# Kernel optimization log

Measured on AMD Instinct MI355X. Metric: run time of the kernel, lower is better.

The kernel has to match this reference:

```python
import jax, jax.numpy as jnp
import numpy as np

NUM_ITERS = 10  # forward() runs power_iteration with num_iters=10


def setup_inputs() -> dict:
    key = jax.random.key(0)
    k1, k2 = jax.random.split(key)
    out_ch, in_ch, h, w = 2048, 2048, 3, 3
    conv_filter = jax.random.normal(k1, (out_ch, in_ch, h, w), dtype=jnp.float32) * 0.02
    u = jax.random.normal(k2, (1, in_ch * w), dtype=jnp.float32)
    u = u / jnp.linalg.norm(u, axis=1, keepdims=True)
    return {"conv_filter": conv_filter, "u": u}


def reference(conv_filter, u):
    out_ch, in_ch, h, w = conv_filter.shape
    # permute (0,2,1,3) then view as [out_ch*h, in_ch*w]
    W = jnp.transpose(conv_filter, (0, 2, 1, 3)).reshape(out_ch * h, in_ch * w)
    Ws = jax.lax.stop_gradient(W)  # power iteration vectors are detached

    def body(i, carry):
        u_n, _ = carry
        v = u_n @ Ws.T                                   # [1, out_ch*h]
        v_n = v / jnp.linalg.norm(v, axis=1, keepdims=True)
        u2 = v_n @ Ws                                    # [1, in_ch*w]
        u_n2 = u2 / jnp.linalg.norm(u2, axis=1, keepdims=True)
        return (u_n2, v_n)

    v0 = jnp.zeros((1, out_ch * h), dtype=conv_filter.dtype)  # overwritten in first iter
    u_n, v_n = jax.lax.fori_loop(0, NUM_ITERS, body, (u, v0))

    # sigma = v W u^T with u, v treated as constants (custom autograd Function)
    sigma = (v_n @ W) @ u_n.T                            # [1, 1]
    return jnp.sqrt(jnp.asarray(h * w, dtype=conv_filter.dtype)) * sigma
```

## Files before the change

### kernel.cpp

```cpp
#include <hip/hip_runtime.h>
#include <hip/hip_bf16.h>
#include <hip/hip_fp16.h>

#define OC_N     2048
#define IC_N     2048
#define RC       6144
#define OCSTRIDE 18432
#define UNSCALE  0.0000152587890625f

typedef float v2f __attribute__((ext_vector_type(2)));

__device__ __forceinline__ float wave_reduce(float x) {
#pragma unroll
    for (int off = 32; off > 0; off >>= 1) x += __shfl_down(x, off, 64);
    return x;
}

__global__ __launch_bounds__(256) void convert_q_kernel(
    const float* __restrict__ conv, unsigned char* __restrict__ Wq)
{
    const int t  = blockIdx.x * 256 + threadIdx.x;
    const int o8 = t * 8;
    const int r  = o8 / RC;
    const int c0 = o8 % RC;
    const int oc = r / 3, hh = r % 3;
    const float* base = conv + (size_t)oc * OCSTRIDE + hh * 3;
    float f[8];
#pragma unroll
    for (int e = 0; e < 8; ++e) {
        const int c  = c0 + e;
        const int ic = c / 3, ww = c - 3 * ic;
        f[e] = base[ic * 9 + ww] * 256.0f;
    }
    int lo = __builtin_amdgcn_cvt_pk_fp8_f32(f[0], f[1], 0, false);
    lo     = __builtin_amdgcn_cvt_pk_fp8_f32(f[2], f[3], lo, true);
    int hi = __builtin_amdgcn_cvt_pk_fp8_f32(f[4], f[5], 0, false);
    hi     = __builtin_amdgcn_cvt_pk_fp8_f32(f[6], f[7], hi, true);
    *reinterpret_cast<uint2*>(Wq + o8) = make_uint2((unsigned)lo, (unsigned)hi);
}

__global__ __launch_bounds__(256) void transpose_q_kernel(
    const unsigned char* __restrict__ Wq, unsigned char* __restrict__ WqT)
{
    __shared__ unsigned char tile[64][68];
    const int tid = threadIdx.x;
    const int tr  = blockIdx.x;
    const int tc  = blockIdx.y;

    const int r  = tid >> 2;
    const int cq = (tid & 3) * 16;
    const uint4 w = *reinterpret_cast<const uint4*>(
        Wq + (size_t)(tr * 64 + r) * RC + tc * 64 + cq);
    *reinterpret_cast<unsigned int*>(&tile[r][cq +  0]) = w.x;
    *reinterpret_cast<unsigned int*>(&tile[r][cq +  4]) = w.y;
    *reinterpret_cast<unsigned int*>(&tile[r][cq +  8]) = w.z;
    *reinterpret_cast<unsigned int*>(&tile[r][cq + 12]) = w.w;
    __syncthreads();

    const int orow = tid >> 2;
    const int ocq  = (tid & 3) * 16;
    unsigned int u32s[4];
#pragma unroll
    for (int wi = 0; wi < 4; ++wi) {
        const int ro = ocq + 4 * wi;
        u32s[wi] =  (unsigned int)tile[ro + 0][orow]
                 | ((unsigned int)tile[ro + 1][orow] << 8)
                 | ((unsigned int)tile[ro + 2][orow] << 16)
                 | ((unsigned int)tile[ro + 3][orow] << 24);
    }
    uint4 o = make_uint4(u32s[0], u32s[1], u32s[2], u32s[3]);
    *reinterpret_cast<uint4*>(WqT + (size_t)(tc * 64 + orow) * RC + tr * 64 + ocq) = o;
}

__device__ __forceinline__ float dot16(uint4 w, float4 a, float4 b, float4 c, float4 d) {
    float acc = 0.f;
    v2f f;
    f = __builtin_amdgcn_cvt_pk_f32_fp8(w.x, false); acc += f.x * a.x + f.y * a.y;
    f = __builtin_amdgcn_cvt_pk_f32_fp8(w.x, true);  acc += f.x * a.z + f.y * a.w;
    f = __builtin_amdgcn_cvt_pk_f32_fp8(w.y, false); acc += f.x * b.x + f.y * b.y;
    f = __builtin_amdgcn_cvt_pk_f32_fp8(w.y, true);  acc += f.x * b.z + f.y * b.w;
    f = __builtin_amdgcn_cvt_pk_f32_fp8(w.z, false); acc += f.x * c.x + f.y * c.y;
    f = __builtin_amdgcn_cvt_pk_f32_fp8(w.z, true);  acc += f.x * c.z + f.y * c.w;
    f = __builtin_amdgcn_cvt_pk_f32_fp8(w.w, false); acc += f.x * d.x + f.y * d.y;
    f = __builtin_amdgcn_cvt_pk_f32_fp8(w.w, true);  acc += f.x * d.z + f.y * d.w;
    return acc;
}

__global__ __launch_bounds__(256) void matvec_q_kernel(
    const unsigned char* __restrict__ W, const float* __restrict__ x,
    float* __restrict__ y, float scale)
{
    const int tid  = threadIdx.x;
    const int lane = tid & 63;
    const int wid  = tid >> 6;
    const int r    = blockIdx.x * 4 + wid;

    const unsigned char* w0 = W + (size_t)r * RC;
    const float4* x4 = reinterpret_cast<const float4*>(x);
    float acc = 0.f;
#pragma unroll
    for (int i = 0; i < 6; ++i) {
        const int c = i * 1024 + lane * 16;
        const uint4 w = *reinterpret_cast<const uint4*>(w0 + c);
        const float4 a = x4[(c >> 2) + 0];
        const float4 b = x4[(c >> 2) + 1];
        const float4 e = x4[(c >> 2) + 2];
        const float4 d = x4[(c >> 2) + 3];
        acc += dot16(w, a, b, e, d);
    }
    acc = wave_reduce(acc);
    if (lane == 0) y[r] = acc * scale;
}

__global__ __launch_bounds__(256) void final_kernel(
    const float* __restrict__ v, const float* __restrict__ t,
    const float* __restrict__ u, float* __restrict__ out)
{
    __shared__ float ssv[4];
    __shared__ float ssu[4];
    __shared__ float sdot[4];
    const int tid  = threadIdx.x;
    const int lane = tid & 63;
    const int wid  = tid >> 6;
    float sqv = 0.f, squ = 0.f, dot = 0.f;
#pragma unroll
    for (int k = 0; k < 24; ++k) {
        const float xv = v[tid + 256 * k];
        const float xt = t[tid + 256 * k];
        const float xu = u[tid + 256 * k];
        sqv += xv * xv;
        squ += xu * xu;
        dot += xv * xt;
    }
    sqv = wave_reduce(sqv);
    squ = wave_reduce(squ);
    dot = wave_reduce(dot);
    if (lane == 0) { ssv[wid] = sqv; ssu[wid] = squ; sdot[wid] = dot; }
    __syncthreads();
    if (tid == 0) {
        const float vs = ssv[0] + ssv[1] + ssv[2] + ssv[3];
        const float us = ssu[0] + ssu[1] + ssu[2] + ssu[3];
        const float dt = sdot[0] + sdot[1] + sdot[2] + sdot[3];
        out[0] = (3.0f / 256.0f) * dt * rsqrtf(vs) * rsqrtf(us);
    }
}

extern "C" void kernel_launch(void* const* d_in, const int* in_sizes, int n_in,
                              void* d_out, int out_size, void* d_ws, size_t ws_size,
                              hipStream_t stream)
{
    const float* conv = (const float*)d_in[0];
    const float* u_in = (const float*)d_in[1];
    float* out = (float*)d_out;

    const size_t WQ_BYTES = (size_t)RC * RC;
    const size_t needed = 2 * WQ_BYTES + (size_t)3 * RC * sizeof(float);
    if (ws_size < needed) return;

    unsigned char* Wq  = (unsigned char*)d_ws;
    unsigned char* WqT = Wq + WQ_BYTES;
    float* v_vec = (float*)(WqT + WQ_BYTES);
    float* u_vec = v_vec + RC;
    float* t_vec = u_vec + RC;

    convert_q_kernel<<<RC * RC / 8 / 256, 256, 0, stream>>>(conv, Wq);
    transpose_q_kernel<<<dim3(RC / 64, RC / 64), 256, 0, stream>>>(Wq, WqT);

    for (int i = 0; i < 10; ++i) {
        matvec_q_kernel<<<RC / 4, 256, 0, stream>>>(
            Wq, (i == 0) ? u_in : u_vec, v_vec, 1.0f);
        matvec_q_kernel<<<RC / 4, 256, 0, stream>>>(
            WqT, v_vec, u_vec, UNSCALE);
    }

    matvec_q_kernel<<<RC / 4, 256, 0, stream>>>(Wq, u_vec, t_vec, 1.0f);
    final_kernel<<<1, 256, 0, stream>>>(v_vec, t_vec, u_vec, out);
}
```

Before: 479.5 us.

## Fuse power-iteration matvecs into one persistent kernel with software grid barriers

Replaces the 21 separate matvec launches with a single persistent kernel of 768 blocks. Each block computes two rows per wave, stages the input vector in padded LDS, and synchronises the grid through an arrival/release barrier in workspace memory. Each iteration writes to its own output buffer, so no buffer is overwritten while another block may still read it. This removes per-launch overhead and gaps between launches, but the kernel relies on all 768 blocks being co-resident, and the barrier adds spin-wait latency and relaxed-ordering risk.

Result: slower. 1.078 ms (+124.7%).

```diff
diff --git a/kernel.cpp b/kernel.cpp
--- a/kernel.cpp
+++ b/kernel.cpp
@@ -7,6 +7,9 @@
 #define RC       6144
 #define OCSTRIDE 18432
 #define UNSCALE  0.0000152587890625f
+#define NBLK     768
+#define NITER    10
+#define SLOT     16
 
 typedef float v2f __attribute__((ext_vector_type(2)));
 
@@ -16,9 +19,24 @@
     return x;
 }
 
+__device__ __forceinline__ void cstore(float* p, float x) {
+    __hip_atomic_store(p, x, __ATOMIC_RELAXED, __HIP_MEMORY_SCOPE_AGENT);
+}
+__device__ __forceinline__ void cstore_i(int* p, int x) {
+    __hip_atomic_store(p, x, __ATOMIC_RELAXED, __HIP_MEMORY_SCOPE_AGENT);
+}
+__device__ __forceinline__ int cload_i(const int* p) {
+    return __hip_atomic_load(const_cast<int*>(p), __ATOMIC_RELAXED,
+                             __HIP_MEMORY_SCOPE_AGENT);
+}
+
 __global__ __launch_bounds__(256) void convert_q_kernel(
-    const float* __restrict__ conv, unsigned char* __restrict__ Wq)
-{
+    const float* __restrict__ conv, unsigned char* __restrict__ Wq,
+    int* __restrict__ barrier_mem)
+{
+    if (blockIdx.x < 2 * NBLK * SLOT / 256) {
+        barrier_mem[blockIdx.x * 256 + threadIdx.x] = 0;
+    }
     const int t  = blockIdx.x * 256 + threadIdx.x;
     const int o8 = t * 8;
     const int r  = o8 / RC;
@@ -86,30 +104,104 @@
     return acc;
 }
 
-__global__ __launch_bounds__(256) void matvec_q_kernel(
-    const unsigned char* __restrict__ W, const float* __restrict__ x,
-    float* __restrict__ y, float scale)
-{
-    const int tid  = threadIdx.x;
-    const int lane = tid & 63;
-    const int wid  = tid >> 6;
-    const int r    = blockIdx.x * 4 + wid;
-
-    const unsigned char* w0 = W + (size_t)r * RC;
-    const float4* x4 = reinterpret_cast<const float4*>(x);
-    float acc = 0.f;
+__device__ __forceinline__ void stage_x(const float* __restrict__ x,
+                                        float4* __restrict__ x4, int tid) {
+    const float4* s4 = reinterpret_cast<const float4*>(x);
+#pragma unroll
+    for (int k = 0; k < 6; ++k) {
+        const int g = tid + 256 * k;
+        x4[g + (g >> 2)] = s4[g];
+    }
+}
+
+__device__ __forceinline__ void matvec_rows2(
+    const unsigned char* __restrict__ W, const float4* __restrict__ x4,
+    int rbase, int lane, float* out0, float* out1)
+{
+    const unsigned char* w0 = W + (size_t)rbase * RC;
+    float acc0 = 0.f, acc1 = 0.f;
 #pragma unroll
     for (int i = 0; i < 6; ++i) {
-        const int c = i * 1024 + lane * 16;
-        const uint4 w = *reinterpret_cast<const uint4*>(w0 + c);
-        const float4 a = x4[(c >> 2) + 0];
-        const float4 b = x4[(c >> 2) + 1];
-        const float4 e = x4[(c >> 2) + 2];
-        const float4 d = x4[(c >> 2) + 3];
-        acc += dot16(w, a, b, e, d);
-    }
-    acc = wave_reduce(acc);
-    if (lane == 0) y[r] = acc * scale;
+        const int slot = i * 320 + lane * 5;
+        const float4 a = x4[slot + 0];
+        const float4 b = x4[slot + 1];
+        const float4 c = x4[slot + 2];
+        const float4 d = x4[slot + 3];
+        const uint4 wA = *reinterpret_cast<const uint4*>(w0 +      i * 1024 + lane * 16);
+        const uint4 wB = *reinterpret_cast<const uint4*>(w0 + RC + i * 1024 + lane * 16);
+        acc0 += dot16(wA, a, b, c, d);
+        acc1 += dot16(wB, a, b, c, d);
+    }
+    *out0 = wave_reduce(acc0);
+    *out1 = wave_reduce(acc1);
+}
+
+__device__ __forceinline__ void grid_barrier(int* __restrict__ arrival,
+                                             int* __restrict__ release,
+                                             int bid, int tid, int g)
+{
+    __syncthreads();
+    if (tid == 0) cstore_i(&arrival[bid * SLOT], g);
+    if (bid == 0) {
+        if (tid < 64) {
+            const int base = tid * 12;
+            for (;;) {
+                bool ok = true;
+#pragma unroll
+                for (int k = 0; k < 12; ++k)
+                    ok &= (cload_i(&arrival[(base + k) * SLOT]) >= g);
+                if (__all(ok)) break;
+                __builtin_amdgcn_s_sleep(1);
+            }
+#pragma unroll
+            for (int k = 0; k < 12; ++k)
+                cstore_i(&release[(base + k) * SLOT], g);
+        }
+    } else if (tid == 0) {
+        while (cload_i(&release[bid * SLOT]) < g)
+            __builtin_amdgcn_s_sleep(1);
+    }
+    __syncthreads();
+}
+
+__global__ __launch_bounds__(256, 3) void power_iter_kernel(
+    const unsigned char* __restrict__ Wq, const unsigned char* __restrict__ WqT,
+    const float* __restrict__ u_in, float* __restrict__ vbufs,
+    float* __restrict__ ubufs, int* __restrict__ barrier_mem)
+{
+    __shared__ float x_lds[7680];
+    float4* x4 = reinterpret_cast<float4*>(x_lds);
+    int* arrival = barrier_mem;
+    int* release = barrier_mem + NBLK * SLOT;
+
+    const int tid   = threadIdx.x;
+    const int lane  = tid & 63;
+    const int wid   = tid >> 6;
+    const int bid   = blockIdx.x;
+    const int rbase = bid * 8 + wid * 2;
+    int g = 0;
+
+    for (int it = 0; it <= NITER; ++it) {
+        const float* src = (it == 0) ? u_in : (ubufs + (size_t)(it - 1) * RC);
+        stage_x(src, x4, tid);
+        __syncthreads();
+        float a0, a1;
+        matvec_rows2(Wq, x4, rbase, lane, &a0, &a1);
+        float* vout = vbufs + (size_t)it * RC;
+        if (lane == 0) { cstore(&vout[rbase], a0); cstore(&vout[rbase + 1], a1); }
+        if (it == NITER) break;
+        ++g; grid_barrier(arrival, release, bid, tid, g);
+
+        stage_x(vout, x4, tid);
+        __syncthreads();
+        matvec_rows2(WqT, x4, rbase, lane, &a0, &a1);
+        float* uout = ubufs + (size_t)it * RC;
+        if (lane == 0) {
+            cstore(&uout[rbase],     a0 * UNSCALE);
+            cstore(&uout[rbase + 1], a1 * UNSCALE);
+        }
+        ++g; grid_barrier(arrival, release, bid, tid, g);
+    }
 }
 
 __global__ __launch_bounds__(256) void final_kernel(
@@ -154,25 +246,23 @@
     float* out = (float*)d_out;
 
     const size_t WQ_BYTES = (size_t)RC * RC;
-    const size_t needed = 2 * WQ_BYTES + (size_t)3 * RC * sizeof(float);
+    const size_t needed = 2 * WQ_BYTES
+                        + (size_t)(2 * NITER + 1) * RC * sizeof(float)
+                        + (size_t)2 * NBLK * SLOT * sizeof(int);
     if (ws_size < needed) return;
 
     unsigned char* Wq  = (unsigned char*)d_ws;
     unsigned char* WqT = Wq + WQ_BYTES;
-    float* v_vec = (float*)(WqT + WQ_BYTES);
-    float* u_vec = v_vec + RC;
-    float* t_vec = u_vec + RC;
-
-    convert_q_kernel<<<RC * RC / 8 / 256, 256, 0, stream>>>(conv, Wq);
+    float* vbufs = (float*)(WqT + WQ_BYTES);
+    float* ubufs = vbufs + (size_t)(NITER + 1) * RC;
+    int*   bmem  = (int*)(ubufs + (size_t)NITER * RC);
+
+    convert_q_kernel<<<RC * RC / 8 / 256, 256, 0, stream>>>(conv, Wq, bmem);
     transpose_q_kernel<<<dim3(RC / 64, RC / 64), 256, 0, stream>>>(Wq, WqT);
-
-    for (int i = 0; i < 10; ++i) {
-        matvec_q_kernel<<<RC / 4, 256, 0, stream>>>(
-            Wq, (i == 0) ? u_in : u_vec, v_vec, 1.0f);
-        matvec_q_kernel<<<RC / 4, 256, 0, stream>>>(
-            WqT, v_vec, u_vec, UNSCALE);
-    }
-
-    matvec_q_kernel<<<RC / 4, 256, 0, stream>>>(Wq, u_vec, t_vec, 1.0f);
-    final_kernel<<<1, 256, 0, stream>>>(v_vec, t_vec, u_vec, out);
-}
+    power_iter_kernel<<<NBLK, 256, 0, stream>>>(Wq, WqT, u_in, vbufs, ubufs, bmem);
+
+    final_kernel<<<1, 256, 0, stream>>>(
+        vbufs + (size_t)(NITER - 1) * RC,
+        vbufs + (size_t)NITER * RC,
+        ubufs + (size_t)(NITER - 1) * RC, out);
+}
```
